# Optimization experiments

Measured on AMD Instinct MI355X. Metric: run time of the kernel, lower is better.

Reference implementation:

```python
import jax, jax.numpy as jnp
import numpy as np


def _fwd_diffs(x, D, scale):
    # forward difference along each of the first D axes, zero at the end, scaled by x.shape[0]
    outs = []
    for d in range(D):
        pad = [(0, 0)] * x.ndim
        pad[d] = (0, 1)
        outs.append(jnp.pad(jnp.diff(x, axis=d), pad) * scale)
    return jnp.stack(outs, 0)


def _bwd_diffs(p, scale):
    # p: [D, *dims, l]; backward difference of p[i] along axis i with the torch narrow/cat semantics
    outs = []
    for i in range(p.shape[0]):
        pi = p[i]
        head = jax.lax.slice_in_dim(pi, 0, pi.shape[i] - 1, axis=i)
        z = jnp.zeros_like(jax.lax.slice_in_dim(pi, 0, 1, axis=i))
        before = jnp.concatenate([head, z], axis=i)
        after = jnp.concatenate([z, head], axis=i)
        outs.append((before - after) * scale)
    return jnp.stack(outs, 0)


def _solver(f, repeats, l, lmbda, nu):
    dims = list(f.shape)
    H = dims[0]
    D = len(dims) - 1
    res = 1.0 / H
    tauu = res / 6.0
    sigmap = res / (3.0 + l)
    sigmas = 1.0
    proj = l * (l - 1) // 2 + l
    tau = 1.0 / (2.0 + proj / 4.0)
    # (k1,k2) interval combinations and the membership matrix M[K,z] = (k1<=z<=k2)
    combos = np.array([(a, b) for a in range(l) for b in range(a, l)], dtype=np.int32)
    k1 = jnp.asarray(combos[:, 0])
    k2 = jnp.asarray(combos[:, 1])
    zz = np.arange(l)
    M = jnp.asarray(((combos[:, :1] <= zz) & (zz <= combos[:, 1:2])).astype(np.float32))  # [proj, l]

    img = jnp.broadcast_to(f[..., None], tuple(dims) + (l,))
    klf = jnp.arange(1, l + 1, dtype=f.dtype) / l - img  # k/l - f
    u = img
    ubar = img
    px = jnp.zeros((D,) + tuple(dims) + (l,), f.dtype)
    pt = jnp.zeros(tuple(dims) + (l,), f.dtype)
    sx = jnp.zeros((D,) + tuple(dims) + (proj,), f.dtype)
    mux = sx
    mubarx = sx
    nrj = jnp.zeros((), f.dtype)
    h_un = u

    for it in range(int(repeats)):
        # ---- parabola: dual ascent on (px,pt) with closed-form cubic (Cardano) projection ----
        musum = jnp.einsum('...p,pz->...z', mux, M)
        ux = px + sigmap * (_fwd_diffs(ubar, D, H) + musum)
        ut = pt + sigmap * (jnp.pad(jnp.diff(ubar, axis=-1), [(0, 0)] * (ubar.ndim - 1) + [(0, 1)]) * l)
        pen = lmbda * klf * klf
        B = 0.25 * jnp.sum(ux * ux, axis=0) - pen
        mask = ut < B
        y = ut + pen
        norm = jnp.sqrt(jnp.sum(ux * ux, axis=0))
        a = 0.5 * norm                                   # 2*0.25*norm
        b = (2.0 / 3.0) * (1.0 - 0.5 * y)
        sb = jnp.sqrt(jnp.maximum(-b, 0.0))              # sqrt(-b), only used where b<0
        d = jnp.where(b < 0, (a - sb ** 3) * (a + sb ** 3), a * a + b ** 3)
        c = jnp.power(a + jnp.sqrt(jnp.maximum(d, 0.0)), 1.0 / 3.0)
        mask1 = (d >= 0) & (c == 0)
        mask3 = d < 0
        sb3 = jnp.where(sb > 0, sb ** 3, 1.0)
        ratio = jnp.clip(a / sb3, -1.0, 1.0)
        c_safe = jnp.where(c == 0, 1.0, c)
        v = jnp.where(mask1, 0.0,
                      jnp.where(mask3, 2.0 * sb * jnp.cos(jnp.arccos(ratio) / 3.0), c - b / c_safe))
        norm_safe = jnp.where(norm == 0, 1.0, norm)
        px = jnp.where(mask[None],
                       jnp.where((norm == 0)[None], 0.0, (2.0 * v / norm_safe)[None] * ux),
                       ux)
        pt = jnp.where(mask, 0.25 * jnp.sum(px * px, axis=0) - pen, ut)

        # ---- l2 projection of s ----
        mx = sx - sigmas * mubarx
        snorm = jnp.sqrt(jnp.sum(mx * mx, axis=0))
        snorm_safe = jnp.where(snorm == 0, 1.0, snorm)
        sx = jnp.where((snorm > nu * H)[None], mx * nu / snorm_safe[None], mx)

        # ---- mu update: per-(k1,k2) partial sums over the label axis via cumsum ----
        cs = jnp.cumsum(px, axis=-1)
        cs = jnp.pad(cs, [(0, 0)] * (px.ndim - 1) + [(1, 0)])
        t = cs[..., k2 + 1] - cs[..., k1]                # [D, *dims, proj]
        mux_new = mux + tau * (sx - t)
        mubarx = 2.0 * mux_new - mux
        mux = mux_new

        # ---- clipping: primal update with box projection and boundary conditions ----
        if it % 10 == 0:
            h_un = u
        dx = _bwd_diffs(px, H)
        head = pt[..., :-1]
        z = jnp.zeros_like(pt[..., :1])
        dt = (jnp.concatenate([head, z], axis=-1) - jnp.concatenate([z, head], axis=-1)) * l
        Dv = u + tauu * (jnp.sum(dx, axis=0) + dt)
        un = jnp.clip(Dv, 0.0, 1.0)
        un = un.at[..., 0].set(1.0).at[..., l - 1].set(0.0)
        ubar = 2.0 * un - u
        u = un
        if it % 10 == 0:
            nrj = jnp.sum(jnp.abs(u - h_un))
    return u, nrj


def setup_inputs() -> dict:
    key = jax.random.key(0)
    H, W = 256, 256
    f = jax.random.uniform(key, (H, W, 1), dtype=jnp.float32)
    return {"f": f, "repeats": 10, "l": 16, "lmbda": 0.5, "nu": 0.1, "tol": 0.0}


def reference(f, repeats, l, lmbda, nu, tol):
    # tol/early-exit: tol=0 so the torch break never fires; iteration count is fixed at `repeats`.
    u, nrj = _solver(f, repeats, l, lmbda, nu)
    denom = float(np.prod(f.shape[:-1])) * l
    return (u, nrj, nrj / denom, 0)
```

## Files before the change

kernel.cpp:

```cpp
#include <hip/hip_runtime.h>

#define HH 256
#define WW 256
#define NPIX (HH*WW)
#define LL 16
#define NL (NPIX*LL)
#define PP 136
#define PP2 (PP*2)

typedef _Float16 half_t;
typedef __attribute__((ext_vector_type(8))) _Float16 half8;

static constexpr float SIGMAP_F = (float)((1.0/256.0)/(3.0+16.0));
static constexpr float TAUU_F   = (float)((1.0/256.0)/6.0);
static constexpr float TAU_F    = (float)(1.0/36.0);

__device__ __forceinline__ float clampf(float x, float lo, float hi){
    return fminf(fmaxf(x, lo), hi);
}

__global__ __launch_bounds__(256) void k_init(const float* __restrict__ f,
    float* __restrict__ u, half_t* __restrict__ ubar, float* __restrict__ nrj)
{
    int tid = blockIdx.x*256 + threadIdx.x;
    if (tid == 0) *nrj = 0.0f;
    if (tid >= NL) return;
    int n = tid >> 4;
    float fv = f[n];
    u[tid]    = fv;
    ubar[tid] = (half_t)fv;
}

__global__ __launch_bounds__(256) void k_prox(const float* __restrict__ f,
    const half_t* __restrict__ ubar,
    const half_t* __restrict__ pxOld,
    half_t* __restrict__ pxCur,
    half_t* __restrict__ pt,
    const half_t* __restrict__ musum)
{
    int tid = blockIdx.x*256 + threadIdx.x;
    if (tid >= NL) return;
    int z = tid & (LL-1);
    int n = tid >> 4;
    int i = n >> 8;
    int j = n & (WW-1);

    float ub = (float)ubar[tid];
    float g0 = (i < HH-1) ? ((float)ubar[tid + WW*LL] - ub) * 256.0f : 0.0f;
    float g1 = (j < WW-1) ? ((float)ubar[tid + LL]    - ub) * 256.0f : 0.0f;
    float gt = (z < LL-1) ? ((float)ubar[tid + 1]     - ub) * 16.0f  : 0.0f;

    float ms0 = (float)musum[tid];
    float ms1 = (float)musum[NL + tid];

    float ux0 = (float)pxOld[tid]      + SIGMAP_F * (g0 + ms0);
    float ux1 = (float)pxOld[NL + tid] + SIGMAP_F * (g1 + ms1);
    float ut  = (float)pt[tid]         + SIGMAP_F * gt;

    float klf = (float)(z + 1) * 0.0625f - f[n];
    float pen = 0.5f * klf * klf;

    float n2 = ux0*ux0 + ux1*ux1;
    float B  = 0.25f * n2 - pen;
    bool mask = ut < B;

    float px0 = ux0, px1 = ux1, ptn = ut;
    if (mask) {
        float y    = ut + pen;
        float norm = sqrtf(n2);
        float a    = 0.5f * norm;
        float b    = (2.0f/3.0f) * (1.0f - 0.5f*y);
        float v;
        if (b < 0.0f) {
            float sb  = sqrtf(-b);
            float sb3 = sb*sb*sb;
            float dd  = (a - sb3)*(a + sb3);
            if (dd < 0.0f) {
                float ratio = clampf(a / sb3, -1.0f, 1.0f);
                v = 2.0f * sb * cosf(acosf(ratio) * (1.0f/3.0f));
            } else {
                float c = cbrtf(a + sqrtf(dd));
                v = (c == 0.0f) ? 0.0f : (c - b/c);
            }
        } else {
            float dd = a*a + b*b*b;
            float c  = cbrtf(a + sqrtf(dd));
            v = (c == 0.0f) ? 0.0f : (c - b/c);
        }
        if (norm == 0.0f) { px0 = 0.0f; px1 = 0.0f; }
        else              { float s = 2.0f*v/norm; px0 = s*ux0; px1 = s*ux1; }
        ptn = 0.25f*(px0*px0 + px1*px1) - pen;
    }
    pxCur[tid]      = (half_t)px0;
    pxCur[NL + tid] = (half_t)px1;
    pt[tid]         = (half_t)ptn;
}

template<int H>
__device__ __forceinline__ void do_set(int d, int n, int lane,
    half8 ph0, half8 ph1, half8 pp0, half8 pp1,
    const half_t* __restrict__ muC,
    half_t* __restrict__ muO,
    float* __restrict__ part)
{
    constexpr size_t setbase = (size_t)H * 17 * 2 * NPIX;
    const size_t vb   = setbase + (size_t)n*16 + (size_t)d*8;
    const size_t vb1  = vb + (size_t)16*NPIX;
    const size_t tail = setbase + (size_t)32*NPIX + (size_t)n*2 + (size_t)d;

    half8 mCv0 = *reinterpret_cast<const half8*>(&muC[vb]);
    half8 mCv1 = *reinterpret_cast<const half8*>(&muC[vb1]);
    half8 mOv0 = *reinterpret_cast<const half8*>(&muO[vb]);
    half8 mOv1 = *reinterpret_cast<const half8*>(&muO[vb1]);
    float mCT = (float)muC[tail];
    float mOT = (float)muO[tail];

    half8 muo0, muo1;
    half_t muoT = (half_t)0.0f;

    float C[LL];
    #pragma unroll
    for (int q = 0; q < LL; ++q) C[q] = 0.0f;

    float tsum = 0.0f, tprev = 0.0f, rsA = 0.0f, rsB = 0.0f;
    #pragma unroll
    for (int q = 0; q < 17; ++q) {
        const int b = (q <= 15-H) ? H + q : q - 1;
        float mC, mO;
        if (q < 8)       { mC=(float)mCv0[q];   mO=(float)mOv0[q]; }
        else if (q < 16) { mC=(float)mCv1[q-8]; mO=(float)mOv1[q-8]; }
        else             { mC=mCT;              mO=mOT; }

        if (q == 0 || q == 16-H) { tsum = 0.0f; tprev = 0.0f; }
        tsum  += (b < 8) ? (float)ph0[b] : (float)ph1[b-8];
        tprev += (b < 8) ? (float)pp0[b] : (float)pp1[b-8];

        float sxp = (mC - mO) * 36.0f + tprev;
        float mx  = sxp - (2.0f*mC - mO);
        float mo  = __shfl_xor(mx, 1);
        float snorm = sqrtf(mx*mx + mo*mo);
        if (snorm > 25.6f) mx *= 0.1f / snorm;
        float mn = mC + TAU_F*(mx - tsum);

        if (q < 8)       muo0[q]   = (half_t)mn;
        else if (q < 16) muo1[q-8] = (half_t)mn;
        else             muoT      = (half_t)mn;

        if (q <= 15-H) rsA += mn; else rsB += mn;
        C[b] += mn;
    }

    *reinterpret_cast<half8*>(&muO[vb])  = muo0;
    *reinterpret_cast<half8*>(&muO[vb1]) = muo1;
    muO[tail] = muoT;

    float m = 0.0f;
    #pragma unroll
    for (int z = 0; z < LL; ++z) {
        if (z == H)    m += rsA;
        if (z == 15-H) m += rsB;
        if (z >= 1)    m -= C[z-1];
        part[H*1024 + z*64 + lane] = m;
    }
}

__global__ __launch_bounds__(512) void k_smu_u(
    const half_t* __restrict__ pxCur,
    const half_t* __restrict__ pxOld,
    const half_t* __restrict__ pt,
    const half_t* __restrict__ muC,
    half_t* __restrict__ muO,
    half_t* __restrict__ musum,
    float* __restrict__ u, half_t* __restrict__ ubar,
    float* __restrict__ nrj, int compute_nrj)
{
    __shared__ float part[8192];
    __shared__ float wsum[8];

    int tid  = threadIdx.x;
    int wv   = tid >> 6;
    int lane = tid & 63;
    int pix  = lane >> 1;
    int d    = lane & 1;
    int n    = blockIdx.x*32 + pix;

    const half8* pv  = reinterpret_cast<const half8*>(pxCur + (size_t)d*NL + (size_t)n*LL);
    const half8* ppv = reinterpret_cast<const half8*>(pxOld + (size_t)d*NL + (size_t)n*LL);
    half8 ph0 = pv[0],  ph1 = pv[1];
    half8 pp0 = ppv[0], pp1 = ppv[1];

    if      (wv == 0) do_set<0>(d,n,lane,ph0,ph1,pp0,pp1,muC,muO,part);
    else if (wv == 1) do_set<1>(d,n,lane,ph0,ph1,pp0,pp1,muC,muO,part);
    else if (wv == 2) do_set<2>(d,n,lane,ph0,ph1,pp0,pp1,muC,muO,part);
    else if (wv == 3) do_set<3>(d,n,lane,ph0,ph1,pp0,pp1,muC,muO,part);
    else if (wv == 4) do_set<4>(d,n,lane,ph0,ph1,pp0,pp1,muC,muO,part);
    else if (wv == 5) do_set<5>(d,n,lane,ph0,ph1,pp0,pp1,muC,muO,part);
    else if (wv == 6) do_set<6>(d,n,lane,ph0,ph1,pp0,pp1,muC,muO,part);
    else              do_set<7>(d,n,lane,ph0,ph1,pp0,pp1,muC,muO,part);

    __syncthreads();

    #pragma unroll
    for (int r = 0; r < 2; ++r) {
        int z2    = (tid >> 6) + r*8;
        int inner = tid & 63;
        float s = 0.0f;
        #pragma unroll
        for (int hh = 0; hh < 8; ++hh) s += part[hh*1024 + z2*64 + inner];
        int d2 = inner & 1, pix2 = inner >> 1;
        musum[(size_t)d2*NL + ((size_t)blockIdx.x*32 + pix2)*LL + z2] = (half_t)s;
    }

    {
        int t  = blockIdx.x*512 + tid;
        int z  = t & (LL-1);
        int n2 = t >> 4;
        int i2 = n2 >> 8;
        int j2 = n2 & (WW-1);

        float p0c = (float)pxCur[t];
        float p1c = (float)pxCur[NL + t];
        float d0 = ((i2 < HH-1) ? p0c : 0.0f) - ((i2 > 0) ? (float)pxCur[t - WW*LL] : 0.0f);
        float d1 = ((j2 < WW-1) ? p1c : 0.0f) - ((j2 > 0) ? (float)pxCur[NL + t - LL] : 0.0f);
        float ptc = (float)pt[t];
        float dt = ((z < LL-1) ? ptc : 0.0f) - ((z > 0) ? (float)pt[t - 1] : 0.0f);

        float uo = u[t];
        float Dv = uo + TAUU_F * ((d0 + d1) * 256.0f + dt * 16.0f);
        float un = clampf(Dv, 0.0f, 1.0f);
        if (z == 0)     un = 1.0f;
        if (z == LL-1)  un = 0.0f;
        u[t]    = un;
        ubar[t] = (half_t)(2.0f*un - uo);

        if (compute_nrj) {
            float v = fabsf(un - uo);
            #pragma unroll
            for (int off = 32; off > 0; off >>= 1) v += __shfl_down(v, off);
            if ((tid & 63) == 0) wsum[wv] = v;
            __syncthreads();
            if (tid == 0) {
                float s = 0.0f;
                #pragma unroll
                for (int q = 0; q < 8; ++q) s += wsum[q];
                atomicAdd(nrj, s);
            }
        }
    }
}

__global__ void k_final(const float* __restrict__ nrj, float* __restrict__ out_tail)
{
    if (threadIdx.x == 0) {
        float e = *nrj;
        out_tail[0] = e;
        out_tail[1] = e * (1.0f/1048576.0f);
        out_tail[2] = 0.0f;
    }
}

extern "C" void kernel_launch(void* const* d_in, const int* in_sizes, int n_in,
                              void* d_out, int out_size, void* d_ws, size_t ws_size,
                              hipStream_t stream)
{
    const float* f = (const float*)d_in[0];
    float* out = (float*)d_out;

    char* w = (char*)d_ws;
    size_t off = 0;
    auto allocf = [&](size_t nfloats) {
        float* p = (float*)(w + off);
        off += nfloats * sizeof(float);
        return p;
    };
    auto alloch = [&](size_t nhalf) {
        half_t* p = (half_t*)(w + off);
        off += nhalf * sizeof(half_t);
        return p;
    };
    half_t* muA    = alloch((size_t)NPIX * PP2);
    half_t* muB    = alloch((size_t)NPIX * PP2);
    half_t* musum  = alloch(2*(size_t)NL);
    half_t* pxA    = alloch(2*(size_t)NL);
    half_t* pxB    = alloch(2*(size_t)NL);
    half_t* pt     = alloch((size_t)NL);
    half_t* ubar   = alloch((size_t)NL);
    size_t half_bytes = off;
    float*  u      = allocf((size_t)NL);
    float*  nrj    = allocf(64);
    (void)ws_size; (void)in_sizes; (void)n_in; (void)out_size;

    hipMemsetAsync(muA, 0, half_bytes, stream);
    k_init<<<NL/256, 256, 0, stream>>>(f, u, ubar, nrj);

    half_t* pxC = pxA;
    half_t* pxO = pxB;
    half_t* mC  = muA;
    half_t* mO  = muB;
    for (int it = 0; it < 10; ++it) {
        k_prox<<<NL/256, 256, 0, stream>>>(f, ubar, pxO, pxC, pt, musum);
        k_smu_u<<<NPIX/32, 512, 0, stream>>>(pxC, pxO, pt, mC, mO, musum,
                                             u, ubar, nrj, it == 0 ? 1 : 0);
        { half_t* tmp = pxC; pxC = pxO; pxO = tmp; }
        { half_t* tmp = mC;  mC  = mO;  mO  = tmp; }
    }

    hipMemcpyAsync(out, u, (size_t)NL*sizeof(float), hipMemcpyDeviceToDevice, stream);
    k_final<<<1, 64, 0, stream>>>(nrj, out + NL);
}
```

Measured before the change: 453.6 us.

## Specialize first iterations to exploit known-zero state and drop init memset

Templates the prox and mu/u kernels on an iteration mode so the first iteration computes directly from f, with px, pt, mu and musum taken as zero, and the second skips loading the older mu buffer, which is still zero. This removes the large workspace memset and the init kernel, along with the redundant loads of zero-valued state in early iterations. It also adds a launch_bounds occupancy hint of 4 on the smu kernel, which may constrain registers. Correctness relies on mode 0 writing every buffer that later iterations read, such as pt and musum.

After: 423.7 us. -6.6%, faster.

```diff
diff --git a/kernel.cpp b/kernel.cpp
--- a/kernel.cpp
+++ b/kernel.cpp
@@ -19,45 +19,44 @@
     return fminf(fmaxf(x, lo), hi);
 }
 
-__global__ __launch_bounds__(256) void k_init(const float* __restrict__ f,
-    float* __restrict__ u, half_t* __restrict__ ubar, float* __restrict__ nrj)
-{
-    int tid = blockIdx.x*256 + threadIdx.x;
-    if (tid == 0) *nrj = 0.0f;
-    if (tid >= NL) return;
-    int n = tid >> 4;
-    float fv = f[n];
-    u[tid]    = fv;
-    ubar[tid] = (half_t)fv;
-}
-
+template<int MODE>
 __global__ __launch_bounds__(256) void k_prox(const float* __restrict__ f,
     const half_t* __restrict__ ubar,
     const half_t* __restrict__ pxOld,
     half_t* __restrict__ pxCur,
     half_t* __restrict__ pt,
-    const half_t* __restrict__ musum)
+    const half_t* __restrict__ musum,
+    float* __restrict__ nrj)
 {
     int tid = blockIdx.x*256 + threadIdx.x;
+    if (MODE == 0 && tid == 0) *nrj = 0.0f;
     if (tid >= NL) return;
     int z = tid & (LL-1);
     int n = tid >> 4;
     int i = n >> 8;
     int j = n & (WW-1);
 
-    float ub = (float)ubar[tid];
-    float g0 = (i < HH-1) ? ((float)ubar[tid + WW*LL] - ub) * 256.0f : 0.0f;
-    float g1 = (j < WW-1) ? ((float)ubar[tid + LL]    - ub) * 256.0f : 0.0f;
-    float gt = (z < LL-1) ? ((float)ubar[tid + 1]     - ub) * 16.0f  : 0.0f;
-
-    float ms0 = (float)musum[tid];
-    float ms1 = (float)musum[NL + tid];
-
-    float ux0 = (float)pxOld[tid]      + SIGMAP_F * (g0 + ms0);
-    float ux1 = (float)pxOld[NL + tid] + SIGMAP_F * (g1 + ms1);
-    float ut  = (float)pt[tid]         + SIGMAP_F * gt;
-
-    float klf = (float)(z + 1) * 0.0625f - f[n];
+    float ux0, ux1, ut;
+    float fv = f[n];
+    if (MODE == 0) {
+        float g0 = (i < HH-1) ? (f[n + WW] - fv) * 256.0f : 0.0f;
+        float g1 = (j < WW-1) ? (f[n + 1]  - fv) * 256.0f : 0.0f;
+        ux0 = SIGMAP_F * g0;
+        ux1 = SIGMAP_F * g1;
+        ut  = 0.0f;
+    } else {
+        float ub = (float)ubar[tid];
+        float g0 = (i < HH-1) ? ((float)ubar[tid + WW*LL] - ub) * 256.0f : 0.0f;
+        float g1 = (j < WW-1) ? ((float)ubar[tid + LL]    - ub) * 256.0f : 0.0f;
+        float gt = (z < LL-1) ? ((float)ubar[tid + 1]     - ub) * 16.0f  : 0.0f;
+        float ms0 = (float)musum[tid];
+        float ms1 = (float)musum[NL + tid];
+        ux0 = (float)pxOld[tid]      + SIGMAP_F * (g0 + ms0);
+        ux1 = (float)pxOld[NL + tid] + SIGMAP_F * (g1 + ms1);
+        ut  = (float)pt[tid]         + SIGMAP_F * gt;
+    }
+
+    float klf = (float)(z + 1) * 0.0625f - fv;
     float pen = 0.5f * klf * klf;
 
     float n2 = ux0*ux0 + ux1*ux1;
@@ -96,7 +95,7 @@
     pt[tid]         = (half_t)ptn;
 }
 
-template<int H>
+template<int H, int MODE>
 __device__ __forceinline__ void do_set(int d, int n, int lane,
     half8 ph0, half8 ph1, half8 pp0, half8 pp1,
     const half_t* __restrict__ muC,
@@ -108,12 +107,18 @@
     const size_t vb1  = vb + (size_t)16*NPIX;
     const size_t tail = setbase + (size_t)32*NPIX + (size_t)n*2 + (size_t)d;
 
-    half8 mCv0 = *reinterpret_cast<const half8*>(&muC[vb]);
-    half8 mCv1 = *reinterpret_cast<const half8*>(&muC[vb1]);
-    half8 mOv0 = *reinterpret_cast<const half8*>(&muO[vb]);
-    half8 mOv1 = *reinterpret_cast<const half8*>(&muO[vb1]);
-    float mCT = (float)muC[tail];
-    float mOT = (float)muO[tail];
+    half8 mCv0, mCv1, mOv0, mOv1;
+    float mCT = 0.0f, mOT = 0.0f;
+    if (MODE >= 1) {
+        mCv0 = *reinterpret_cast<const half8*>(&muC[vb]);
+        mCv1 = *reinterpret_cast<const half8*>(&muC[vb1]);
+        mCT  = (float)muC[tail];
+    }
+    if (MODE == 2) {
+        mOv0 = *reinterpret_cast<const half8*>(&muO[vb]);
+        mOv1 = *reinterpret_cast<const half8*>(&muO[vb1]);
+        mOT  = (float)muO[tail];
+    }
 
     half8 muo0, muo1;
     half_t muoT = (half_t)0.0f;
@@ -126,21 +131,26 @@
     #pragma unroll
     for (int q = 0; q < 17; ++q) {
         const int b = (q <= 15-H) ? H + q : q - 1;
-        float mC, mO;
-        if (q < 8)       { mC=(float)mCv0[q];   mO=(float)mOv0[q]; }
-        else if (q < 16) { mC=(float)mCv1[q-8]; mO=(float)mOv1[q-8]; }
-        else             { mC=mCT;              mO=mOT; }
-
         if (q == 0 || q == 16-H) { tsum = 0.0f; tprev = 0.0f; }
         tsum  += (b < 8) ? (float)ph0[b] : (float)ph1[b-8];
-        tprev += (b < 8) ? (float)pp0[b] : (float)pp1[b-8];
-
-        float sxp = (mC - mO) * 36.0f + tprev;
-        float mx  = sxp - (2.0f*mC - mO);
-        float mo  = __shfl_xor(mx, 1);
-        float snorm = sqrtf(mx*mx + mo*mo);
-        if (snorm > 25.6f) mx *= 0.1f / snorm;
-        float mn = mC + TAU_F*(mx - tsum);
+
+        float mn;
+        if (MODE == 0) {
+            mn = -TAU_F * tsum;
+        } else {
+            float mC, mO = 0.0f;
+            if (q < 8)       { mC=(float)mCv0[q];   if (MODE==2) mO=(float)mOv0[q]; }
+            else if (q < 16) { mC=(float)mCv1[q-8]; if (MODE==2) mO=(float)mOv1[q-8]; }
+            else             { mC=mCT;              if (MODE==2) mO=mOT; }
+            tprev += (b < 8) ? (float)pp0[b] : (float)pp1[b-8];
+
+            float sxp = (mC - mO) * 36.0f + tprev;
+            float mx  = sxp - (2.0f*mC - mO);
+            float mo  = __shfl_xor(mx, 1);
+            float snorm = sqrtf(mx*mx + mo*mo);
+            if (snorm > 25.6f) mx *= 0.1f / snorm;
+            mn = mC + TAU_F*(mx - tsum);
+        }
 
         if (q < 8)       muo0[q]   = (half_t)mn;
         else if (q < 16) muo1[q-8] = (half_t)mn;
@@ -164,7 +174,9 @@
     }
 }
 
-__global__ __launch_bounds__(512) void k_smu_u(
+template<int MODE>
+__global__ __launch_bounds__(512, 4) void k_smu_u(
+    const float* __restrict__ f,
     const half_t* __restrict__ pxCur,
     const half_t* __restrict__ pxOld,
     const half_t* __restrict__ pt,
@@ -172,7 +184,7 @@
     half_t* __restrict__ muO,
     half_t* __restrict__ musum,
     float* __restrict__ u, half_t* __restrict__ ubar,
-    float* __restrict__ nrj, int compute_nrj)
+    float* __restrict__ nrj)
 {
     __shared__ float part[8192];
     __shared__ float wsum[8];
@@ -184,19 +196,22 @@
     int d    = lane & 1;
     int n    = blockIdx.x*32 + pix;
 
-    const half8* pv  = reinterpret_cast<const half8*>(pxCur + (size_t)d*NL + (size_t)n*LL);
-    const half8* ppv = reinterpret_cast<const half8*>(pxOld + (size_t)d*NL + (size_t)n*LL);
-    half8 ph0 = pv[0],  ph1 = pv[1];
-    half8 pp0 = ppv[0], pp1 = ppv[1];
-
-    if      (wv == 0) do_set<0>(d,n,lane,ph0,ph1,pp0,pp1,muC,muO,part);
-    else if (wv == 1) do_set<1>(d,n,lane,ph0,ph1,pp0,pp1,muC,muO,part);
-    else if (wv == 2) do_set<2>(d,n,lane,ph0,ph1,pp0,pp1,muC,muO,part);
-    else if (wv == 3) do_set<3>(d,n,lane,ph0,ph1,pp0,pp1,muC,muO,part);
-    else if (wv == 4) do_set<4>(d,n,lane,ph0,ph1,pp0,pp1,muC,muO,part);
-    else if (wv == 5) do_set<5>(d,n,lane,ph0,ph1,pp0,pp1,muC,muO,part);
-    else if (wv == 6) do_set<6>(d,n,lane,ph0,ph1,pp0,pp1,muC,muO,part);
-    else              do_set<7>(d,n,lane,ph0,ph1,pp0,pp1,muC,muO,part);
+    const half8* pv = reinterpret_cast<const half8*>(pxCur + (size_t)d*NL + (size_t)n*LL);
+    half8 ph0 = pv[0], ph1 = pv[1];
+    half8 pp0, pp1;
+    if (MODE >= 1) {
+        const half8* ppv = reinterpret_cast<const half8*>(pxOld + (size_t)d*NL + (size_t)n*LL);
+        pp0 = ppv[0]; pp1 = ppv[1];
+    }
+
+    if      (wv == 0) do_set<0,MODE>(d,n,lane,ph0,ph1,pp0,pp1,muC,muO,part);
+    else if (wv == 1) do_set<1,MODE>(d,n,lane,ph0,ph1,pp0,pp1,muC,muO,part);
+    else if (wv == 2) do_set<2,MODE>(d,n,lane,ph0,ph1,pp0,pp1,muC,muO,part);
+    else if (wv == 3) do_set<3,MODE>(d,n,lane,ph0,ph1,pp0,pp1,muC,muO,part);
+    else if (wv == 4) do_set<4,MODE>(d,n,lane,ph0,ph1,pp0,pp1,muC,muO,part);
+    else if (wv == 5) do_set<5,MODE>(d,n,lane,ph0,ph1,pp0,pp1,muC,muO,part);
+    else if (wv == 6) do_set<6,MODE>(d,n,lane,ph0,ph1,pp0,pp1,muC,muO,part);
+    else              do_set<7,MODE>(d,n,lane,ph0,ph1,pp0,pp1,muC,muO,part);
 
     __syncthreads();
 
@@ -225,7 +240,7 @@
         float ptc = (float)pt[t];
         float dt = ((z < LL-1) ? ptc : 0.0f) - ((z > 0) ? (float)pt[t - 1] : 0.0f);
 
-        float uo = u[t];
+        float uo = (MODE == 0) ? f[n2] : u[t];
         float Dv = uo + TAUU_F * ((d0 + d1) * 256.0f + dt * 16.0f);
         float un = clampf(Dv, 0.0f, 1.0f);
         if (z == 0)     un = 1.0f;
@@ -233,7 +248,7 @@
         u[t]    = un;
         ubar[t] = (half_t)(2.0f*un - uo);
 
-        if (compute_nrj) {
+        if (MODE == 0) {
             float v = fabsf(un - uo);
             #pragma unroll
             for (int off = 32; off > 0; off >>= 1) v += __shfl_down(v, off);
@@ -285,22 +300,25 @@
     half_t* pxB    = alloch(2*(size_t)NL);
     half_t* pt     = alloch((size_t)NL);
     half_t* ubar   = alloch((size_t)NL);
-    size_t half_bytes = off;
     float*  u      = allocf((size_t)NL);
     float*  nrj    = allocf(64);
     (void)ws_size; (void)in_sizes; (void)n_in; (void)out_size;
-
-    hipMemsetAsync(muA, 0, half_bytes, stream);
-    k_init<<<NL/256, 256, 0, stream>>>(f, u, ubar, nrj);
 
     half_t* pxC = pxA;
     half_t* pxO = pxB;
     half_t* mC  = muA;
     half_t* mO  = muB;
     for (int it = 0; it < 10; ++it) {
-        k_prox<<<NL/256, 256, 0, stream>>>(f, ubar, pxO, pxC, pt, musum);
-        k_smu_u<<<NPIX/32, 512, 0, stream>>>(pxC, pxO, pt, mC, mO, musum,
-                                             u, ubar, nrj, it == 0 ? 1 : 0);
+        if (it == 0) {
+            k_prox<0><<<NL/256, 256, 0, stream>>>(f, ubar, pxO, pxC, pt, musum, nrj);
+            k_smu_u<0><<<NPIX/32, 512, 0, stream>>>(f, pxC, pxO, pt, mC, mO, musum, u, ubar, nrj);
+        } else if (it == 1) {
+            k_prox<1><<<NL/256, 256, 0, stream>>>(f, ubar, pxO, pxC, pt, musum, nrj);
+            k_smu_u<1><<<NPIX/32, 512, 0, stream>>>(f, pxC, pxO, pt, mC, mO, musum, u, ubar, nrj);
+        } else {
+            k_prox<1><<<NL/256, 256, 0, stream>>>(f, ubar, pxO, pxC, pt, musum, nrj);
+            k_smu_u<2><<<NPIX/32, 512, 0, stream>>>(f, pxC, pxO, pt, mC, mO, musum, u, ubar, nrj);
+        }
         { half_t* tmp = pxC; pxC = pxO; pxO = tmp; }
         { half_t* tmp = mC;  mC  = mO;  mO  = tmp; }
     }
```
